# Kernel optimization log

Hardware: AMD Instinct MI355X
Metric: run time of the kernel (lower is better)

Reference implementation:

```python
import jax, jax.numpy as jnp
import numpy as np

B, S, HID = 2, 2048, 1024
H, HKV, D = 16, 8, 128
G = H // HKV  # GQA group size
EPS = 1e-6
THETA = 1000000.0


def setup_inputs() -> dict:
    key = jax.random.key(0)
    ks = jax.random.split(key, 6)
    hidden_states = jax.random.normal(ks[0], (B, S, HID), dtype=jnp.float32)
    # causal boolean mask: True = attend
    attention_mask = jnp.tril(jnp.ones((S, S), dtype=bool))[None, None]
    # RoPE tables (HF convention: freqs duplicated across both halves)
    inv_freq = 1.0 / (THETA ** (jnp.arange(0, D, 2, dtype=jnp.float32) / D))
    ang = jnp.arange(S, dtype=jnp.float32)[:, None] * inv_freq[None, :]  # [S, D/2]
    emb = jnp.concatenate([ang, ang], axis=-1)  # [S, D]
    cos, sin = jnp.cos(emb), jnp.sin(emb)
    std = 0.02
    Wq = jax.random.normal(ks[1], (HID, H * D), dtype=jnp.float32) * std
    Wk = jax.random.normal(ks[2], (HID, HKV * D), dtype=jnp.float32) * std
    Wv = jax.random.normal(ks[3], (HID, HKV * D), dtype=jnp.float32) * std
    Wo = jax.random.normal(ks[4], (H * D, HID), dtype=jnp.float32) * std
    q_norm_w = jnp.ones((D,), dtype=jnp.float32)
    k_norm_w = jnp.ones((D,), dtype=jnp.float32)
    return {"hidden_states": hidden_states, "attention_mask": attention_mask,
            "cos": cos, "sin": sin, "Wq": Wq, "Wk": Wk, "Wv": Wv, "Wo": Wo,
            "q_norm_w": q_norm_w, "k_norm_w": k_norm_w}


def _rms_norm(x, w):
    var = jnp.mean(x * x, axis=-1, keepdims=True)
    return x * jax.lax.rsqrt(var + EPS) * w


def _rotate_half(x):
    x1, x2 = jnp.split(x, 2, axis=-1)
    return jnp.concatenate([-x2, x1], axis=-1)


def reference(hidden_states, attention_mask, cos, sin, Wq, Wk, Wv, Wo, q_norm_w, k_norm_w):
    b, s, _ = hidden_states.shape
    xq = (hidden_states @ Wq).reshape(b, s, H, D).transpose(0, 2, 1, 3)    # [B,H,S,D]
    xk = (hidden_states @ Wk).reshape(b, s, HKV, D).transpose(0, 2, 1, 3)  # [B,Hkv,S,D]
    xv = (hidden_states @ Wv).reshape(b, s, HKV, D).transpose(0, 2, 1, 3)  # [B,Hkv,S,D]
    xq = _rms_norm(xq, q_norm_w)
    xk = _rms_norm(xk, k_norm_w)
    c = cos[None, None]  # [1,1,S,D]
    si = sin[None, None]
    xq = xq * c + _rotate_half(xq) * si
    xk = xk * c + _rotate_half(xk) * si
    # GQA without materializing repeated KV: group q heads per kv head
    xqg = xq.reshape(b, HKV, G, s, D)
    scale = 1.0 / jnp.sqrt(jnp.asarray(D, dtype=xq.dtype))
    scores = jnp.einsum('bkgsd,bktd->bkgst', xqg, xk) * scale  # [B,Hkv,G,S,S]
    mask = attention_mask[:, :, None]  # [1,1,1,S,S]
    scores = jnp.where(mask, scores, jnp.asarray(-jnp.inf, dtype=scores.dtype))
    probs = jax.nn.softmax(scores, axis=-1)
    out = jnp.einsum('bkgst,bktd->bkgsd', probs, xv)  # [B,Hkv,G,S,D]
    out = out.reshape(b, H, s, D).transpose(0, 2, 1, 3).reshape(b, s, H * D)
    return out @ Wo
```

## Files before the change

kernel.cpp:

```cpp
#include <hip/hip_runtime.h>
#include <stdint.h>

#define B_ 2
#define S_ 2048
#define H_ 16
#define HKV_ 8
#define D_ 128
#define EPS_ 1e-6f
#define SCALE_ 0.08838834764831845f

typedef __attribute__((ext_vector_type(8))) __bf16 bf16x8;
typedef __attribute__((ext_vector_type(4))) float f32x4;
typedef __attribute__((ext_vector_type(16))) float f32x16;

static __device__ __forceinline__ uint16_t f2b(float f) {
  uint32_t u = __builtin_bit_cast(uint32_t, f);
  u += 0x7fffu + ((u >> 16) & 1u);
  return (uint16_t)(u >> 16);
}
static __device__ __forceinline__ float b2f(uint16_t b) {
  uint32_t u = ((uint32_t)b) << 16;
  return __builtin_bit_cast(float, u);
}

typedef const __attribute__((address_space(1))) uint32_t* gas_p;
typedef __attribute__((address_space(3))) uint32_t* las_p;
static __device__ __forceinline__ void gload16(const void* g, void* l) {
  __builtin_amdgcn_global_load_lds((gas_p)g, (las_p)l, 16, 0, 0);
}

__global__ __launch_bounds__(256) void prep(const float* __restrict__ hidden,
                                            uint16_t* __restrict__ Xb,
                                            const float* __restrict__ Wq,
                                            const float* __restrict__ Wk,
                                            const float* __restrict__ Wv,
                                            const float* __restrict__ Wo,
                                            uint16_t* __restrict__ Wqt,
                                            uint16_t* __restrict__ Wkt,
                                            uint16_t* __restrict__ Wvt,
                                            uint16_t* __restrict__ Wot) {
  __shared__ float tt[32][33];
  int bid = blockIdx.x;
  if (bid < 4096) {
    int i = bid * 256 + threadIdx.x;
    float4 f = ((const float4*)hidden)[i];
    uint2 o;
    o.x = (uint32_t)f2b(f.x) | ((uint32_t)f2b(f.y) << 16);
    o.y = (uint32_t)f2b(f.z) | ((uint32_t)f2b(f.w) << 16);
    ((uint2*)Xb)[i] = o;
    return;
  }
  bid -= 4096;
  const float* src; uint16_t* dst; int K, N, bx, by;
  if (bid < 2048)       { src = Wq; dst = Wqt; K = 1024; N = 2048; bx = bid & 63; by = bid >> 6; }
  else if (bid < 3072)  { bid -= 2048; src = Wk; dst = Wkt; K = 1024; N = 1024; bx = bid & 31; by = bid >> 5; }
  else if (bid < 4096)  { bid -= 3072; src = Wv; dst = Wvt; K = 1024; N = 1024; bx = bid & 31; by = bid >> 5; }
  else                  { bid -= 4096; src = Wo; dst = Wot; K = 2048; N = 1024; bx = bid & 31; by = bid >> 5; }
  int nb = bx * 32, kb = by * 32;
  int tx = threadIdx.x & 31, ty = threadIdx.x >> 5;
  #pragma unroll
  for (int i = ty; i < 32; i += 8) tt[i][tx] = src[(size_t)(kb + i) * N + nb + tx];
  __syncthreads();
  #pragma unroll
  for (int i = ty; i < 32; i += 8) dst[(size_t)(nb + i) * K + kb + tx] = f2b(tt[tx][i]);
}

__global__ __launch_bounds__(256) void gemm_qkv(const uint16_t* __restrict__ A,
                                                const uint16_t* __restrict__ Bt,
                                                uint16_t* __restrict__ Qb,
                                                uint16_t* __restrict__ Kb,
                                                uint16_t* __restrict__ Vtb,
                                                const float* __restrict__ qw,
                                                const float* __restrict__ kw,
                                                const float* __restrict__ cosr,
                                                const float* __restrict__ sinr) {
  __shared__ uint16_t Sh[128 * 128];
  uint16_t* Al = Sh;
  uint16_t* Bl = Sh + 128 * 64;
  int tid = threadIdx.x;
  int lane = tid & 63, lr = lane & 15, g = lane >> 4;
  int w = tid >> 6, wm = w >> 1, wn = w & 1;
  int wbase = w * 64;
  int m0 = blockIdx.y * 128, n0 = blockIdx.x * 128;
  f32x4 acc[4][4] = {};
  for (int k0 = 0; k0 < 1024; k0 += 64) {
    __syncthreads();
    #pragma unroll
    for (int p = 0; p < 4; ++p) {
      int c = tid + p * 256;
      int row = c >> 3, cb = c & 7;
      int sc = (cb ^ (row & 7)) * 8;
      gload16(A + (size_t)(m0 + row) * 1024 + k0 + sc, Al + (size_t)(p * 256 + wbase) * 8);
      gload16(Bt + (size_t)(n0 + row) * 1024 + k0 + sc, Bl + (size_t)(p * 256 + wbase) * 8);
    }
    __syncthreads();
    #pragma unroll
    for (int ks = 0; ks < 2; ++ks) {
      bf16x8 af[4], bfr[4];
      #pragma unroll
      for (int mi = 0; mi < 4; ++mi) {
        int row = wm * 64 + mi * 16 + lr;
        af[mi] = *(bf16x8*)((char*)Al + row * 128 + ((ks * 64 + g * 16) ^ ((row & 7) << 4)));
      }
      #pragma unroll
      for (int ni = 0; ni < 4; ++ni) {
        int row = wn * 64 + ni * 16 + lr;
        bfr[ni] = *(bf16x8*)((char*)Bl + row * 128 + ((ks * 64 + g * 16) ^ ((row & 7) << 4)));
      }
      __builtin_amdgcn_s_setprio(1);
      #pragma unroll
      for (int mi = 0; mi < 4; ++mi)
        #pragma unroll
        for (int ni = 0; ni < 4; ++ni)
          acc[mi][ni] = __builtin_amdgcn_mfma_f32_16x16x32_bf16(af[mi], bfr[ni], acc[mi][ni], 0, 0, 0);
      __builtin_amdgcn_s_setprio(0);
    }
  }
  __syncthreads();
  uint16_t* L = Sh;
  #pragma unroll
  for (int mi = 0; mi < 4; ++mi)
    #pragma unroll
    for (int ni = 0; ni < 4; ++ni)
      #pragma unroll
      for (int e = 0; e < 4; ++e) {
        int row = wm * 64 + mi * 16 + 4 * g + e;
        int col = wn * 64 + ni * 16 + lr;
        L[row * 128 + ((((col >> 3) ^ (row & 7)) << 3) | (col & 7))] = f2b(acc[mi][ni][e]);
      }
  __syncthreads();
  int hsel = n0 >> 7;
  if (hsel < 24) {
    int row = tid >> 1, half = tid & 1;
    int gr = m0 + row, bb = gr >> 11, s = gr & 2047;
    int d0 = half * 32;
    float x[64];
    #pragma unroll
    for (int c8 = 0; c8 < 8; ++c8) {
      int j = (c8 & 3) * 8 + d0 + (c8 >> 2) * 64;
      union { bf16x8 v; uint16_t u[8]; } tmp;
      tmp.v = *(bf16x8*)(L + row * 128 + (((j >> 3) ^ (row & 7)) << 3));
      #pragma unroll
      for (int k = 0; k < 8; ++k) x[c8 * 8 + k] = b2f(tmp.u[k]);
    }
    float ss = 0.f;
    #pragma unroll
    for (int k = 0; k < 64; ++k) ss += x[k] * x[k];
    ss += __shfl_xor(ss, 1, 64);
    float rn = rsqrtf(ss * (1.0f / 128.0f) + EPS_);
    const float* wv = (hsel < 16) ? qw : kw;
    float scq = (hsel < 16) ? SCALE_ : 1.0f;
    rn *= scq;
    uint16_t* outp = (hsel < 16)
      ? Qb + (((size_t)(bb * 16 + hsel)) * 2048 + s) * 128
      : Kb + (((size_t)(bb * 8 + (hsel - 16))) * 2048 + s) * 128;
    const float* cR = cosr + s * 128;
    const float* sR = sinr + s * 128;
    #pragma unroll
    for (int c = 0; c < 4; ++c) {
      int dlo = d0 + c * 8;
      uint16_t olo[8], ohi[8];
      #pragma unroll
      for (int k = 0; k < 8; ++k) {
        int d = dlo + k;
        float x1 = x[c * 8 + k] * rn * wv[d];
        float x2 = x[32 + c * 8 + k] * rn * wv[d + 64];
        olo[k] = f2b(x1 * cR[d] - x2 * sR[d]);
        ohi[k] = f2b(x2 * cR[d + 64] + x1 * sR[d + 64]);
      }
      *(uint4*)(outp + dlo) = *(uint4*)olo;
      *(uint4*)(outp + 64 + dlo) = *(uint4*)ohi;
    }
  } else {
    int kvh = hsel - 24;
    int d0 = tid >> 1, sh = tid & 1;
    int bb = m0 >> 11, sg0 = (m0 & 2047) + sh * 64;
    union { uint16_t u[64]; uint4 q[8]; } vv;
    #pragma unroll
    for (int sl = 0; sl < 64; ++sl) {
      int srow = sh * 64 + sl;
      vv.u[sl] = L[srow * 128 + ((((d0 >> 3) ^ (srow & 7)) << 3) | (d0 & 7))];
    }
    uint16_t* vt = Vtb + (((size_t)(bb * 8 + kvh)) * 128 + d0) * 2048 + sg0;
    #pragma unroll
    for (int c = 0; c < 8; ++c) *(uint4*)(vt + c * 8) = vv.q[c];
  }
}

__global__ __launch_bounds__(256) void gemm_o(const uint16_t* __restrict__ A,
                                              const uint16_t* __restrict__ Bt,
                                              float* __restrict__ Cout,
                                              int M, int N, int K) {
  __shared__ uint16_t Al[128 * 64];
  __shared__ uint16_t Bl[64 * 64];
  int tid = threadIdx.x;
  int lane = tid & 63, lr = lane & 15, g = lane >> 4;
  int w = tid >> 6, wm = w >> 1, wn = w & 1;
  int wbase = w * 64;
  int m0 = blockIdx.y * 128, n0 = blockIdx.x * 64;
  f32x4 acc[4][2] = {};
  for (int k0 = 0; k0 < K; k0 += 64) {
    __syncthreads();
    #pragma unroll
    for (int p = 0; p < 4; ++p) {
      int c = tid + p * 256;
      int row = c >> 3, cb = c & 7;
      int sc = (cb ^ (row & 7)) * 8;
      gload16(A + (size_t)(m0 + row) * K + k0 + sc, Al + (size_t)(p * 256 + wbase) * 8);
    }
    #pragma unroll
    for (int p = 0; p < 2; ++p) {
      int c = tid + p * 256;
      int row = c >> 3, cb = c & 7;
      int sc = (cb ^ (row & 7)) * 8;
      gload16(Bt + (size_t)(n0 + row) * K + k0 + sc, Bl + (size_t)(p * 256 + wbase) * 8);
    }
    __syncthreads();
    #pragma unroll
    for (int ks = 0; ks < 2; ++ks) {
      bf16x8 af[4], bfr[2];
      #pragma unroll
      for (int mi = 0; mi < 4; ++mi) {
        int row = wm * 64 + mi * 16 + lr;
        af[mi] = *(bf16x8*)((char*)Al + row * 128 + ((ks * 64 + g * 16) ^ ((row & 7) << 4)));
      }
      #pragma unroll
      for (int ni = 0; ni < 2; ++ni) {
        int row = wn * 32 + ni * 16 + lr;
        bfr[ni] = *(bf16x8*)((char*)Bl + row * 128 + ((ks * 64 + g * 16) ^ ((row & 7) << 4)));
      }
      __builtin_amdgcn_s_setprio(1);
      #pragma unroll
      for (int mi = 0; mi < 4; ++mi)
        #pragma unroll
        for (int ni = 0; ni < 2; ++ni)
          acc[mi][ni] = __builtin_amdgcn_mfma_f32_16x16x32_bf16(af[mi], bfr[ni], acc[mi][ni], 0, 0, 0);
      __builtin_amdgcn_s_setprio(0);
    }
  }
  #pragma unroll
  for (int mi = 0; mi < 4; ++mi)
    #pragma unroll
    for (int ni = 0; ni < 2; ++ni)
      #pragma unroll
      for (int e = 0; e < 4; ++e) {
        int row = m0 + wm * 64 + mi * 16 + 4 * g + e;
        int col = n0 + wn * 32 + ni * 16 + lr;
        Cout[(size_t)row * N + col] = acc[mi][ni][e];
      }
}

#define STAGE(BUF, KB) {                                                       \
  int kb64 = (KB) * 64;                                                        \
  _Pragma("unroll") for (int p2 = 0; p2 < 4; ++p2) {                           \
    int ck = p2 * 4 + w;                                                       \
    int krow = ck * 4 + (lane >> 4);                                           \
    int kg = (lane & 15) ^ (krow & 7);                                         \
    gload16(Kg + (size_t)(kb64 + krow) * D_ + kg * 8, Kl[BUF] + ck * 512);     \
    int vrow = ck * 8 + (lane >> 3);                                           \
    int vg = (lane & 7) ^ (vrow & 7);                                          \
    gload16(Vg + (size_t)vrow * S_ + kb64 + vg * 8, Vl[BUF] + ck * 512);       \
  } }

__global__ __launch_bounds__(256, 2) void attn_kernel(const uint16_t* __restrict__ Qb,
                                                      const uint16_t* __restrict__ Kb,
                                                      const uint16_t* __restrict__ Vtg,
                                                      uint16_t* __restrict__ out) {
  __shared__ uint16_t Kl[2][64 * 128];
  __shared__ uint16_t Vl[2][128 * 64];
  int tid = threadIdx.x, lane = tid & 63, w = tid >> 6;
  int ql = lane & 31, hi = lane >> 5;
  int bi = blockIdx.x;
  int biH = bi >> 8;
  int j = bi & 255;
  int qgl = j >> 5;
  int qg = biH ? qgl : 15 - qgl;
  int rem = j & 31;
  int bkv = rem >> 1, hsel = rem & 1;
  int b = bkv >> 3, kv = bkv & 7, h = kv * 2 + hsel;
  int qt = qg * 4 + w;
  int q0 = qt * 32;
  int mykb = qt >> 1;
  int kbmax = 2 * qg + 1;
  const uint16_t* Qg = Qb + ((size_t)(b * H_ + h)) * S_ * D_;
  const uint16_t* Kg = Kb + ((size_t)(b * HKV_ + kv)) * S_ * D_;
  const uint16_t* Vg = Vtg + ((size_t)(b * HKV_ + kv)) * S_ * D_;
  bf16x8 qf[8];
  #pragma unroll
  for (int t = 0; t < 8; ++t)
    qf[t] = *(const bf16x8*)(Qg + (size_t)(q0 + ql) * D_ + t * 16 + 8 * hi);
  f32x16 O[4] = {};
  float mrun = -__builtin_inff();
  float lrun = 0.f;
  STAGE(0, 0)
  for (int kb = 0; kb <= kbmax; ++kb) {
    int cur = kb & 1;
    __syncthreads();
    if (kb < kbmax) STAGE(cur ^ 1, kb + 1)
    if (kb <= mykb) {
      const uint16_t* KlC = Kl[cur];
      const uint16_t* VlC = Vl[cur];
      bool diag = (kb == mykb);
      bool skip2 = diag && ((qt & 1) == 0);
      float p0[16], p1[16];
      {
        bf16x8 kf[8];
        #pragma unroll
        for (int t = 0; t < 8; ++t)
          kf[t] = *(const bf16x8*)(KlC + ql * 128 + (((2 * t + hi) ^ (ql & 7)) * 8));
        f32x16 acc = {};
        __builtin_amdgcn_s_setprio(1);
        #pragma unroll
        for (int t = 0; t < 8; ++t)
          acc = __builtin_amdgcn_mfma_f32_32x32x16_bf16(kf[t], qf[t], acc, 0, 0, 0);
        __builtin_amdgcn_s_setprio(0);
        #pragma unroll
        for (int r = 0; r < 16; ++r) p0[r] = acc[r];
      }
      if (!skip2) {
        bf16x8 kf[8];
        #pragma unroll
        for (int t = 0; t < 8; ++t)
          kf[t] = *(const bf16x8*)(KlC + (32 + ql) * 128 + (((2 * t + hi) ^ (ql & 7)) * 8));
        f32x16 acc = {};
        __builtin_amdgcn_s_setprio(1);
        #pragma unroll
        for (int t = 0; t < 8; ++t)
          acc = __builtin_amdgcn_mfma_f32_32x32x16_bf16(kf[t], qf[t], acc, 0, 0, 0);
        __builtin_amdgcn_s_setprio(0);
        #pragma unroll
        for (int r = 0; r < 16; ++r) p1[r] = acc[r];
      }
      if (diag && !(qt & 1)) {
        #pragma unroll
        for (int r = 0; r < 16; ++r) {
          int kk = kb * 64 + 8 * (r >> 2) + 4 * hi + (r & 3);
          if (kk > q0 + ql) p0[r] = -__builtin_inff();
        }
      }
      if (diag && (qt & 1)) {
        #pragma unroll
        for (int r = 0; r < 16; ++r) {
          int kk = kb * 64 + 32 + 8 * (r >> 2) + 4 * hi + (r & 3);
          if (kk > q0 + ql) p1[r] = -__builtin_inff();
        }
      }
      float m8[8];
      #pragma unroll
      for (int i = 0; i < 8; ++i) m8[i] = fmaxf(p0[i], p0[i + 8]);
      if (!skip2) {
        #pragma unroll
        for (int i = 0; i < 8; ++i) m8[i] = fmaxf(m8[i], fmaxf(p1[i], p1[i + 8]));
      }
      float m4a = fmaxf(m8[0], m8[4]), m4b = fmaxf(m8[1], m8[5]);
      float m4c = fmaxf(m8[2], m8[6]), m4d = fmaxf(m8[3], m8[7]);
      float pmax = fmaxf(fmaxf(m4a, m4b), fmaxf(m4c, m4d));
      pmax = fmaxf(pmax, __shfl_xor(pmax, 32, 64));
      if (__any(pmax > mrun + 8.f)) {
        float mnew = fmaxf(mrun, pmax);
        float rs = __expf(mrun - mnew);
        lrun *= rs;
        #pragma unroll
        for (int r = 0; r < 16; ++r) {
          float rr = __shfl(rs, (r & 3) + 8 * (r >> 2) + 4 * hi, 64);
          #pragma unroll
          for (int dt = 0; dt < 4; ++dt) O[dt][r] *= rr;
        }
        mrun = mnew;
      }
      float ls = 0.f;
      union PW { uint32_t w[4]; bf16x8 v; } pa0, pa1;
      #pragma unroll
      for (int r = 0; r < 16; ++r) { p0[r] = __expf(p0[r] - mrun); ls += p0[r]; }
      {
        uint32_t uu[4][2];
        #pragma unroll
        for (int T = 0; T < 4; ++T) {
          asm("v_cvt_pk_bf16_f32 %0, %1, %2" : "=v"(uu[T][0]) : "v"(p0[4 * T]), "v"(p0[4 * T + 1]));
          asm("v_cvt_pk_bf16_f32 %0, %1, %2" : "=v"(uu[T][1]) : "v"(p0[4 * T + 2]), "v"(p0[4 * T + 3]));
        }
        uint32_t a = uu[0][0], bb2 = uu[1][0];
        asm("v_permlane32_swap_b32 %0, %1" : "+v"(a), "+v"(bb2));
        uint32_t c = uu[0][1], d = uu[1][1];
        asm("v_permlane32_swap_b32 %0, %1" : "+v"(c), "+v"(d));
        pa0.w[0] = a; pa0.w[1] = c; pa0.w[2] = bb2; pa0.w[3] = d;
        uint32_t a2 = uu[2][0], b2 = uu[3][0];
        asm("v_permlane32_swap_b32 %0, %1" : "+v"(a2), "+v"(b2));
        uint32_t c2 = uu[2][1], d2 = uu[3][1];
        asm("v_permlane32_swap_b32 %0, %1" : "+v"(c2), "+v"(d2));
        pa1.w[0] = a2; pa1.w[1] = c2; pa1.w[2] = b2; pa1.w[3] = d2;
      }
      __builtin_amdgcn_s_setprio(1);
      #pragma unroll
      for (int dt = 0; dt < 4; ++dt) {
        bf16x8 v0 = *(const bf16x8*)(VlC + (dt * 32 + ql) * 64 + (((0 + hi) ^ (ql & 7)) * 8));
        bf16x8 v1 = *(const bf16x8*)(VlC + (dt * 32 + ql) * 64 + (((2 + hi) ^ (ql & 7)) * 8));
        O[dt] = __builtin_amdgcn_mfma_f32_32x32x16_bf16(pa0.v, v0, O[dt], 0, 0, 0);
        O[dt] = __builtin_amdgcn_mfma_f32_32x32x16_bf16(pa1.v, v1, O[dt], 0, 0, 0);
      }
      __builtin_amdgcn_s_setprio(0);
      if (!skip2) {
        union PW pa2, pa3;
        #pragma unroll
        for (int r = 0; r < 16; ++r) { p1[r] = __expf(p1[r] - mrun); ls += p1[r]; }
        {
          uint32_t uu[4][2];
          #pragma unroll
          for (int T = 0; T < 4; ++T) {
            asm("v_cvt_pk_bf16_f32 %0, %1, %2" : "=v"(uu[T][0]) : "v"(p1[4 * T]), "v"(p1[4 * T + 1]));
            asm("v_cvt_pk_bf16_f32 %0, %1, %2" : "=v"(uu[T][1]) : "v"(p1[4 * T + 2]), "v"(p1[4 * T + 3]));
          }
          uint32_t a = uu[0][0], bb2 = uu[1][0];
          asm("v_permlane32_swap_b32 %0, %1" : "+v"(a), "+v"(bb2));
          uint32_t c = uu[0][1], d = uu[1][1];
          asm("v_permlane32_swap_b32 %0, %1" : "+v"(c), "+v"(d));
          pa2.w[0] = a; pa2.w[1] = c; pa2.w[2] = bb2; pa2.w[3] = d;
          uint32_t a2 = uu[2][0], b2 = uu[3][0];
          asm("v_permlane32_swap_b32 %0, %1" : "+v"(a2), "+v"(b2));
          uint32_t c2 = uu[2][1], d2 = uu[3][1];
          asm("v_permlane32_swap_b32 %0, %1" : "+v"(c2), "+v"(d2));
          pa3.w[0] = a2; pa3.w[1] = c2; pa3.w[2] = b2; pa3.w[3] = d2;
        }
        __builtin_amdgcn_s_setprio(1);
        #pragma unroll
        for (int dt = 0; dt < 4; ++dt) {
          bf16x8 v2 = *(const bf16x8*)(VlC + (dt * 32 + ql) * 64 + (((4 + hi) ^ (ql & 7)) * 8));
          bf16x8 v3 = *(const bf16x8*)(VlC + (dt * 32 + ql) * 64 + (((6 + hi) ^ (ql & 7)) * 8));
          O[dt] = __builtin_amdgcn_mfma_f32_32x32x16_bf16(pa2.v, v2, O[dt], 0, 0, 0);
          O[dt] = __builtin_amdgcn_mfma_f32_32x32x16_bf16(pa3.v, v3, O[dt], 0, 0, 0);
        }
        __builtin_amdgcn_s_setprio(0);
      }
      ls += __shfl_xor(ls, 32, 64);
      lrun += ls;
    }
  }
  float linv = 1.0f / lrun;
  #pragma unroll
  for (int r = 0; r < 16; ++r) {
    int qrl = (r & 3) + 8 * (r >> 2) + 4 * hi;
    float lr_ = __shfl(linv, qrl, 64);
    #pragma unroll
    for (int dt = 0; dt < 4; ++dt) {
      size_t o = ((size_t)(b * S_ + q0 + qrl)) * 2048 + h * 128 + dt * 32 + ql;
      out[o] = f2b(O[dt][r] * lr_);
    }
  }
}

extern "C" void kernel_launch(void* const* d_in, const int* in_sizes, int n_in,
                              void* d_out, int out_size, void* d_ws, size_t ws_size,
                              hipStream_t stream) {
  const float* hidden = (const float*)d_in[0];
  const float* cosr = (const float*)d_in[2];
  const float* sinr = (const float*)d_in[3];
  const float* Wq = (const float*)d_in[4];
  const float* Wk = (const float*)d_in[5];
  const float* Wv = (const float*)d_in[6];
  const float* Wo = (const float*)d_in[7];
  const float* qw = (const float*)d_in[8];
  const float* kw = (const float*)d_in[9];

  uint16_t* p = (uint16_t*)d_ws;
  uint16_t* Xb   = p; p += (size_t)4096 * 1024;
  uint16_t* Wqt  = p; p += (size_t)2048 * 1024;
  uint16_t* Wkt  = p; p += (size_t)1024 * 1024;
  uint16_t* Wvt  = p; p += (size_t)1024 * 1024;
  uint16_t* Wot  = p; p += (size_t)1024 * 2048;
  uint16_t* Qbuf = p; p += (size_t)B_ * H_ * S_ * D_;
  uint16_t* Kbuf = p; p += (size_t)B_ * HKV_ * S_ * D_;
  uint16_t* Vtb  = p; p += (size_t)B_ * HKV_ * S_ * D_;
  uint16_t* attn = p; p += (size_t)4096 * 2048;

  prep<<<10240, 256, 0, stream>>>(hidden, Xb, Wq, Wk, Wv, Wo, Wqt, Wkt, Wvt, Wot);
  gemm_qkv<<<dim3(32, 32), 256, 0, stream>>>(Xb, Wqt, Qbuf, Kbuf, Vtb, qw, kw, cosr, sinr);
  attn_kernel<<<512, 256, 0, stream>>>(Qbuf, Kbuf, Vtb, attn);
  gemm_o<<<dim3(16, 32), 256, 0, stream>>>(attn, Wot, (float*)d_out, 4096, 1024, 2048);
}
```

Measured before the change: 174.9 us.

## Pre-pack K/V into MFMA fragment order and drop LDS staging in attention

```diff
diff --git a/kernel.cpp b/kernel.cpp
--- a/kernel.cpp
+++ b/kernel.cpp
@@ -8,6 +8,7 @@
 #define D_ 128
 #define EPS_ 1e-6f
 #define SCALE_ 0.08838834764831845f
+#define KVSTRIDE_ 262144
 
 typedef __attribute__((ext_vector_type(8))) __bf16 bf16x8;
 typedef __attribute__((ext_vector_type(4))) float f32x4;
@@ -68,8 +69,8 @@
 __global__ __launch_bounds__(256) void gemm_qkv(const uint16_t* __restrict__ A,
                                                 const uint16_t* __restrict__ Bt,
                                                 uint16_t* __restrict__ Qb,
-                                                uint16_t* __restrict__ Kb,
-                                                uint16_t* __restrict__ Vtb,
+                                                uint16_t* __restrict__ Kp,
+                                                uint16_t* __restrict__ Vp,
                                                 const float* __restrict__ qw,
                                                 const float* __restrict__ kw,
                                                 const float* __restrict__ cosr,
@@ -137,9 +138,9 @@
     float x[64];
     #pragma unroll
     for (int c8 = 0; c8 < 8; ++c8) {
-      int j = (c8 & 3) * 8 + d0 + (c8 >> 2) * 64;
+      int jj = (c8 & 3) * 8 + d0 + (c8 >> 2) * 64;
       union { bf16x8 v; uint16_t u[8]; } tmp;
-      tmp.v = *(bf16x8*)(L + row * 128 + (((j >> 3) ^ (row & 7)) << 3));
+      tmp.v = *(bf16x8*)(L + row * 128 + (((jj >> 3) ^ (row & 7)) << 3));
       #pragma unroll
       for (int k = 0; k < 8; ++k) x[c8 * 8 + k] = b2f(tmp.u[k]);
     }
@@ -151,25 +152,46 @@
     const float* wv = (hsel < 16) ? qw : kw;
     float scq = (hsel < 16) ? SCALE_ : 1.0f;
     rn *= scq;
-    uint16_t* outp = (hsel < 16)
-      ? Qb + (((size_t)(bb * 16 + hsel)) * 2048 + s) * 128
-      : Kb + (((size_t)(bb * 8 + (hsel - 16))) * 2048 + s) * 128;
     const float* cR = cosr + s * 128;
     const float* sR = sinr + s * 128;
-    #pragma unroll
-    for (int c = 0; c < 4; ++c) {
-      int dlo = d0 + c * 8;
-      uint16_t olo[8], ohi[8];
-      #pragma unroll
-      for (int k = 0; k < 8; ++k) {
-        int d = dlo + k;
-        float x1 = x[c * 8 + k] * rn * wv[d];
-        float x2 = x[32 + c * 8 + k] * rn * wv[d + 64];
-        olo[k] = f2b(x1 * cR[d] - x2 * sR[d]);
-        ohi[k] = f2b(x2 * cR[d + 64] + x1 * sR[d + 64]);
-      }
-      *(uint4*)(outp + dlo) = *(uint4*)olo;
-      *(uint4*)(outp + 64 + dlo) = *(uint4*)ohi;
+    if (hsel < 16) {
+      uint16_t* outp = Qb + (((size_t)(bb * 16 + hsel)) * 2048 + s) * 128;
+      #pragma unroll
+      for (int c = 0; c < 4; ++c) {
+        int dlo = d0 + c * 8;
+        uint16_t olo[8], ohi[8];
+        #pragma unroll
+        for (int k = 0; k < 8; ++k) {
+          int d = dlo + k;
+          float x1 = x[c * 8 + k] * rn * wv[d];
+          float x2 = x[32 + c * 8 + k] * rn * wv[d + 64];
+          olo[k] = f2b(x1 * cR[d] - x2 * sR[d]);
+          ohi[k] = f2b(x2 * cR[d + 64] + x1 * sR[d + 64]);
+        }
+        *(uint4*)(outp + dlo) = *(uint4*)olo;
+        *(uint4*)(outp + 64 + dlo) = *(uint4*)ohi;
+      }
+    } else {
+      uint16_t* kp = Kp + (size_t)(bb * 8 + (hsel - 16)) * KVSTRIDE_;
+      int kb32 = s >> 5, sl = s & 31;
+      #pragma unroll
+      for (int c = 0; c < 4; ++c) {
+        int dlo = d0 + c * 8;
+        uint16_t olo[8], ohi[8];
+        #pragma unroll
+        for (int k = 0; k < 8; ++k) {
+          int d = dlo + k;
+          float x1 = x[c * 8 + k] * rn * wv[d];
+          float x2 = x[32 + c * 8 + k] * rn * wv[d + 64];
+          olo[k] = f2b(x1 * cR[d] - x2 * sR[d]);
+          ohi[k] = f2b(x2 * cR[d + 64] + x1 * sR[d + 64]);
+        }
+        int ta = dlo >> 4, ha = (dlo >> 3) & 1;
+        *(uint4*)(kp + (((size_t)kb32 * 8 + ta) * 64 + ha * 32 + sl) * 8) = *(uint4*)olo;
+        int dhi = dlo + 64;
+        int tb = dhi >> 4, hb = (dhi >> 3) & 1;
+        *(uint4*)(kp + (((size_t)kb32 * 8 + tb) * 64 + hb * 32 + sl) * 8) = *(uint4*)ohi;
+      }
     }
   } else {
     int kvh = hsel - 24;
@@ -181,9 +203,14 @@
       int srow = sh * 64 + sl;
       vv.u[sl] = L[srow * 128 + ((((d0 >> 3) ^ (srow & 7)) << 3) | (d0 & 7))];
     }
-    uint16_t* vt = Vtb + (((size_t)(bb * 8 + kvh)) * 128 + d0) * 2048 + sg0;
-    #pragma unroll
-    for (int c = 0; c < 8; ++c) *(uint4*)(vt + c * 8) = vv.q[c];
+    uint16_t* vp = Vp + (size_t)(bb * 8 + kvh) * KVSTRIDE_;
+    int dt = d0 >> 5, qlv = d0 & 31;
+    #pragma unroll
+    for (int c = 0; c < 8; ++c) {
+      int s8 = sg0 + c * 8;
+      int kb64 = s8 >> 6, j = (s8 & 63) >> 4, hh = (s8 >> 3) & 1;
+      *(uint4*)(vp + ((((size_t)kb64 * 16) + dt * 4 + j) * 64 + hh * 32 + qlv) * 8) = vv.q[c];
+    }
   }
 }
 
@@ -250,41 +277,21 @@
       }
 }
 
-#define STAGE(BUF, KB) {                                                       \
-  int kb64 = (KB) * 64;                                                        \
-  _Pragma("unroll") for (int p2 = 0; p2 < 4; ++p2) {                           \
-    int ck = p2 * 4 + w;                                                       \
-    int krow = ck * 4 + (lane >> 4);                                           \
-    int kg = (lane & 15) ^ (krow & 7);                                         \
-    gload16(Kg + (size_t)(kb64 + krow) * D_ + kg * 8, Kl[BUF] + ck * 512);     \
-    int vrow = ck * 8 + (lane >> 3);                                           \
-    int vg = (lane & 7) ^ (vrow & 7);                                          \
-    gload16(Vg + (size_t)vrow * S_ + kb64 + vg * 8, Vl[BUF] + ck * 512);       \
-  } }
-
-__global__ __launch_bounds__(256, 2) void attn_kernel(const uint16_t* __restrict__ Qb,
-                                                      const uint16_t* __restrict__ Kb,
-                                                      const uint16_t* __restrict__ Vtg,
-                                                      uint16_t* __restrict__ out) {
-  __shared__ uint16_t Kl[2][64 * 128];
-  __shared__ uint16_t Vl[2][128 * 64];
-  int tid = threadIdx.x, lane = tid & 63, w = tid >> 6;
-  int ql = lane & 31, hi = lane >> 5;
-  int bi = blockIdx.x;
-  int biH = bi >> 8;
-  int j = bi & 255;
-  int qgl = j >> 5;
-  int qg = biH ? qgl : 15 - qgl;
-  int rem = j & 31;
-  int bkv = rem >> 1, hsel = rem & 1;
-  int b = bkv >> 3, kv = bkv & 7, h = kv * 2 + hsel;
-  int qt = qg * 4 + w;
-  int q0 = qt * 32;
-  int mykb = qt >> 1;
-  int kbmax = 2 * qg + 1;
+__global__ __launch_bounds__(64, 2) void attn_kernel(const uint16_t* __restrict__ Qb,
+                                                     const uint16_t* __restrict__ Kp,
+                                                     const uint16_t* __restrict__ Vp,
+                                                     uint16_t* __restrict__ out) {
+  int lane = threadIdx.x & 63, ql = lane & 31, hi = lane >> 5;
+  int wid = blockIdx.x;
+  int x = wid & 7, rest = wid >> 3;
+  int gsel = rest & 1, hsel = (rest >> 1) & 1, qidx = rest >> 2;
+  int gkv = gsel * 8 + x;
+  int b = gkv >> 3, kv = gkv & 7, h = kv * 2 + hsel;
+  int qt = 63 - qidx;
+  int q0 = qt * 32, mykb = qt >> 1;
   const uint16_t* Qg = Qb + ((size_t)(b * H_ + h)) * S_ * D_;
-  const uint16_t* Kg = Kb + ((size_t)(b * HKV_ + kv)) * S_ * D_;
-  const uint16_t* Vg = Vtg + ((size_t)(b * HKV_ + kv)) * S_ * D_;
+  const uint16_t* Kpg = Kp + (size_t)(b * HKV_ + kv) * KVSTRIDE_;
+  const uint16_t* Vpg = Vp + (size_t)(b * HKV_ + kv) * KVSTRIDE_;
   bf16x8 qf[8];
   #pragma unroll
   for (int t = 0; t < 8; ++t)
@@ -292,148 +299,151 @@
   f32x16 O[4] = {};
   float mrun = -__builtin_inff();
   float lrun = 0.f;
-  STAGE(0, 0)
-  for (int kb = 0; kb <= kbmax; ++kb) {
-    int cur = kb & 1;
-    __syncthreads();
-    if (kb < kbmax) STAGE(cur ^ 1, kb + 1)
-    if (kb <= mykb) {
-      const uint16_t* KlC = Kl[cur];
-      const uint16_t* VlC = Vl[cur];
-      bool diag = (kb == mykb);
-      bool skip2 = diag && ((qt & 1) == 0);
-      float p0[16], p1[16];
-      {
-        bf16x8 kf[8];
-        #pragma unroll
-        for (int t = 0; t < 8; ++t)
-          kf[t] = *(const bf16x8*)(KlC + ql * 128 + (((2 * t + hi) ^ (ql & 7)) * 8));
-        f32x16 acc = {};
-        __builtin_amdgcn_s_setprio(1);
-        #pragma unroll
-        for (int t = 0; t < 8; ++t)
-          acc = __builtin_amdgcn_mfma_f32_32x32x16_bf16(kf[t], qf[t], acc, 0, 0, 0);
-        __builtin_amdgcn_s_setprio(0);
-        #pragma unroll
-        for (int r = 0; r < 16; ++r) p0[r] = acc[r];
-      }
-      if (!skip2) {
-        bf16x8 kf[8];
-        #pragma unroll
-        for (int t = 0; t < 8; ++t)
-          kf[t] = *(const bf16x8*)(KlC + (32 + ql) * 128 + (((2 * t + hi) ^ (ql & 7)) * 8));
-        f32x16 acc = {};
-        __builtin_amdgcn_s_setprio(1);
-        #pragma unroll
-        for (int t = 0; t < 8; ++t)
-          acc = __builtin_amdgcn_mfma_f32_32x32x16_bf16(kf[t], qf[t], acc, 0, 0, 0);
-        __builtin_amdgcn_s_setprio(0);
-        #pragma unroll
-        for (int r = 0; r < 16; ++r) p1[r] = acc[r];
-      }
-      if (diag && !(qt & 1)) {
-        #pragma unroll
-        for (int r = 0; r < 16; ++r) {
-          int kk = kb * 64 + 8 * (r >> 2) + 4 * hi + (r & 3);
-          if (kk > q0 + ql) p0[r] = -__builtin_inff();
-        }
-      }
-      if (diag && (qt & 1)) {
-        #pragma unroll
-        for (int r = 0; r < 16; ++r) {
-          int kk = kb * 64 + 32 + 8 * (r >> 2) + 4 * hi + (r & 3);
-          if (kk > q0 + ql) p1[r] = -__builtin_inff();
-        }
-      }
-      float m8[8];
-      #pragma unroll
-      for (int i = 0; i < 8; ++i) m8[i] = fmaxf(p0[i], p0[i + 8]);
-      if (!skip2) {
-        #pragma unroll
-        for (int i = 0; i < 8; ++i) m8[i] = fmaxf(m8[i], fmaxf(p1[i], p1[i + 8]));
-      }
-      float m4a = fmaxf(m8[0], m8[4]), m4b = fmaxf(m8[1], m8[5]);
-      float m4c = fmaxf(m8[2], m8[6]), m4d = fmaxf(m8[3], m8[7]);
-      float pmax = fmaxf(fmaxf(m4a, m4b), fmaxf(m4c, m4d));
-      pmax = fmaxf(pmax, __shfl_xor(pmax, 32, 64));
-      if (__any(pmax > mrun + 8.f)) {
-        float mnew = fmaxf(mrun, pmax);
-        float rs = __expf(mrun - mnew);
-        lrun *= rs;
-        #pragma unroll
-        for (int r = 0; r < 16; ++r) {
-          float rr = __shfl(rs, (r & 3) + 8 * (r >> 2) + 4 * hi, 64);
-          #pragma unroll
-          for (int dt = 0; dt < 4; ++dt) O[dt][r] *= rr;
-        }
-        mrun = mnew;
-      }
-      float ls = 0.f;
-      union PW { uint32_t w[4]; bf16x8 v; } pa0, pa1;
-      #pragma unroll
-      for (int r = 0; r < 16; ++r) { p0[r] = __expf(p0[r] - mrun); ls += p0[r]; }
+  for (int kb = 0; kb <= mykb; ++kb) {
+    bool diag = (kb == mykb);
+    bool skip2 = diag && ((qt & 1) == 0);
+    const uint16_t* Kb64 = Kpg + (size_t)kb * 8192;
+    const uint16_t* Vb64 = Vpg + (size_t)kb * 8192;
+    float p0[16], p1[16];
+    {
+      bf16x8 kf[8];
+      #pragma unroll
+      for (int t = 0; t < 8; ++t)
+        kf[t] = *(const bf16x8*)(Kb64 + (t * 64 + lane) * 8);
+      f32x16 acc = {};
+      __builtin_amdgcn_s_setprio(1);
+      #pragma unroll
+      for (int t = 0; t < 8; ++t)
+        acc = __builtin_amdgcn_mfma_f32_32x32x16_bf16(kf[t], qf[t], acc, 0, 0, 0);
+      __builtin_amdgcn_s_setprio(0);
+      #pragma unroll
+      for (int r = 0; r < 16; ++r) p0[r] = acc[r];
+    }
+    if (!skip2) {
+      bf16x8 kf[8];
+      #pragma unroll
+      for (int t = 0; t < 8; ++t)
+        kf[t] = *(const bf16x8*)(Kb64 + 4096 + (t * 64 + lane) * 8);
+      f32x16 acc = {};
+      __builtin_amdgcn_s_setprio(1);
+      #pragma unroll
+      for (int t = 0; t < 8; ++t)
+        acc = __builtin_amdgcn_mfma_f32_32x32x16_bf16(kf[t], qf[t], acc, 0, 0, 0);
+      __builtin_amdgcn_s_setprio(0);
+      #pragma unroll
+      for (int r = 0; r < 16; ++r) p1[r] = acc[r];
+    }
+    bf16x8 vf[16];
+    #pragma unroll
+    for (int dt = 0; dt < 4; ++dt) {
+      vf[dt * 4 + 0] = *(const bf16x8*)(Vb64 + ((dt * 4 + 0) * 64 + lane) * 8);
+      vf[dt * 4 + 1] = *(const bf16x8*)(Vb64 + ((dt * 4 + 1) * 64 + lane) * 8);
+    }
+    if (!skip2) {
+      #pragma unroll
+      for (int dt = 0; dt < 4; ++dt) {
+        vf[dt * 4 + 2] = *(const bf16x8*)(Vb64 + ((dt * 4 + 2) * 64 + lane) * 8);
+        vf[dt * 4 + 3] = *(const bf16x8*)(Vb64 + ((dt * 4 + 3) * 64 + lane) * 8);
+      }
+    }
+    if (diag && !(qt & 1)) {
+      #pragma unroll
+      for (int r = 0; r < 16; ++r) {
+        int kk = kb * 64 + 8 * (r >> 2) + 4 * hi + (r & 3);
+        if (kk > q0 + ql) p0[r] = -__builtin_inff();
+      }
+    }
+    if (diag && (qt & 1)) {
+      #pragma unroll
+      for (int r = 0; r < 16; ++r) {
+        int kk = kb * 64 + 32 + 8 * (r >> 2) + 4 * hi + (r & 3);
+        if (kk > q0 + ql) p1[r] = -__builtin_inff();
+      }
+    }
+    float m8[8];
+    #pragma unroll
+    for (int i = 0; i < 8; ++i) m8[i] = fmaxf(p0[i], p0[i + 8]);
+    if (!skip2) {
+      #pragma unroll
+      for (int i = 0; i < 8; ++i) m8[i] = fmaxf(m8[i], fmaxf(p1[i], p1[i + 8]));
+    }
+    float m4a = fmaxf(m8[0], m8[4]), m4b = fmaxf(m8[1], m8[5]);
+    float m4c = fmaxf(m8[2], m8[6]), m4d = fmaxf(m8[3], m8[7]);
+    float pmax = fmaxf(fmaxf(m4a, m4b), fmaxf(m4c, m4d));
+    pmax = fmaxf(pmax, __shfl_xor(pmax, 32, 64));
+    if (__any(pmax > mrun + 8.f)) {
+      float mnew = fmaxf(mrun, pmax);
+      float rs = __expf(mrun - mnew);
+      lrun *= rs;
+      #pragma unroll
+      for (int r = 0; r < 16; ++r) {
+        float rr = __shfl(rs, (r & 3) + 8 * (r >> 2) + 4 * hi, 64);
+        #pragma unroll
+        for (int dt = 0; dt < 4; ++dt) O[dt][r] *= rr;
+      }
+      mrun = mnew;
+    }
+    float ls = 0.f;
+    union PW { uint32_t w[4]; bf16x8 v; } pa0, pa1;
+    #pragma unroll
+    for (int r = 0; r < 16; ++r) { p0[r] = __expf(p0[r] - mrun); ls += p0[r]; }
+    {
+      uint32_t uu[4][2];
+      #pragma unroll
+      for (int T = 0; T < 4; ++T) {
+        asm("v_cvt_pk_bf16_f32 %0, %1, %2" : "=v"(uu[T][0]) : "v"(p0[4 * T]), "v"(p0[4 * T + 1]));
+        asm("v_cvt_pk_bf16_f32 %0, %1, %2" : "=v"(uu[T][1]) : "v"(p0[4 * T + 2]), "v"(p0[4 * T + 3]));
+      }
+      uint32_t a = uu[0][0], bb2 = uu[1][0];
+      asm("v_permlane32_swap_b32 %0, %1" : "+v"(a), "+v"(bb2));
+      uint32_t c = uu[0][1], d = uu[1][1];
+      asm("v_permlane32_swap_b32 %0, %1" : "+v"(c), "+v"(d));
+      pa0.w[0] = a; pa0.w[1] = c; pa0.w[2] = bb2; pa0.w[3] = d;
+      uint32_t a2 = uu[2][0], b2 = uu[3][0];
+      asm("v_permlane32_swap_b32 %0, %1" : "+v"(a2), "+v"(b2));
+      uint32_t c2 = uu[2][1], d2 = uu[3][1];
+      asm("v_permlane32_swap_b32 %0, %1" : "+v"(c2), "+v"(d2));
+      pa1.w[0] = a2; pa1.w[1] = c2; pa1.w[2] = b2; pa1.w[3] = d2;
+    }
+    __builtin_amdgcn_s_setprio(1);
+    #pragma unroll
+    for (int dt = 0; dt < 4; ++dt) {
+      O[dt] = __builtin_amdgcn_mfma_f32_32x32x16_bf16(pa0.v, vf[dt * 4 + 0], O[dt], 0, 0, 0);
+      O[dt] = __builtin_amdgcn_mfma_f32_32x32x16_bf16(pa1.v, vf[dt * 4 + 1], O[dt], 0, 0, 0);
+    }
+    __builtin_amdgcn_s_setprio(0);
+    if (!skip2) {
+      union PW pa2, pa3;
+      #pragma unroll
+      for (int r = 0; r < 16; ++r) { p1[r] = __expf(p1[r] - mrun); ls += p1[r]; }
       {
         uint32_t uu[4][2];
         #pragma unroll
         for (int T = 0; T < 4; ++T) {
-          asm("v_cvt_pk_bf16_f32 %0, %1, %2" : "=v"(uu[T][0]) : "v"(p0[4 * T]), "v"(p0[4 * T + 1]));
-          asm("v_cvt_pk_bf16_f32 %0, %1, %2" : "=v"(uu[T][1]) : "v"(p0[4 * T + 2]), "v"(p0[4 * T + 3]));
+          asm("v_cvt_pk_bf16_f32 %0, %1, %2" : "=v"(uu[T][0]) : "v"(p1[4 * T]), "v"(p1[4 * T + 1]));
+          asm("v_cvt_pk_bf16_f32 %0, %1, %2" : "=v"(uu[T][1]) : "v"(p1[4 * T + 2]), "v"(p1[4 * T + 3]));
         }
         uint32_t a = uu[0][0], bb2 = uu[1][0];
         asm("v_permlane32_swap_b32 %0, %1" : "+v"(a), "+v"(bb2));
         uint32_t c = uu[0][1], d = uu[1][1];
         asm("v_permlane32_swap_b32 %0, %1" : "+v"(c), "+v"(d));
-        pa0.w[0] = a; pa0.w[1] = c; pa0.w[2] = bb2; pa0.w[3] = d;
+        pa2.w[0] = a; pa2.w[1] = c; pa2.w[2] = bb2; pa2.w[3] = d;
         uint32_t a2 = uu[2][0], b2 = uu[3][0];
         asm("v_permlane32_swap_b32 %0, %1" : "+v"(a2), "+v"(b2));
         uint32_t c2 = uu[2][1], d2 = uu[3][1];
         asm("v_permlane32_swap_b32 %0, %1" : "+v"(c2), "+v"(d2));
-        pa1.w[0] = a2; pa1.w[1] = c2; pa1.w[2] = b2; pa1.w[3] = d2;
+        pa3.w[0] = a2; pa3.w[1] = c2; pa3.w[2] = b2; pa3.w[3] = d2;
       }
       __builtin_amdgcn_s_setprio(1);
       #pragma unroll
       for (int dt = 0; dt < 4; ++dt) {
-        bf16x8 v0 = *(const bf16x8*)(VlC + (dt * 32 + ql) * 64 + (((0 + hi) ^ (ql & 7)) * 8));
-        bf16x8 v1 = *(const bf16x8*)(VlC + (dt * 32 + ql) * 64 + (((2 + hi) ^ (ql & 7)) * 8));
-        O[dt] = __builtin_amdgcn_mfma_f32_32x32x16_bf16(pa0.v, v0, O[dt], 0, 0, 0);
-        O[dt] = __builtin_amdgcn_mfma_f32_32x32x16_bf16(pa1.v, v1, O[dt], 0, 0, 0);
+        O[dt] = __builtin_amdgcn_mfma_f32_32x32x16_bf16(pa2.v, vf[dt * 4 + 2], O[dt], 0, 0, 0);
+        O[dt] = __builtin_amdgcn_mfma_f32_32x32x16_bf16(pa3.v, vf[dt * 4 + 3], O[dt], 0, 0, 0);
       }
       __builtin_amdgcn_s_setprio(0);
-      if (!skip2) {
-        union PW pa2, pa3;
-        #pragma unroll
-        for (int r = 0; r < 16; ++r) { p1[r] = __expf(p1[r] - mrun); ls += p1[r]; }
-        {
-          uint32_t uu[4][2];
-          #pragma unroll
-          for (int T = 0; T < 4; ++T) {
-            asm("v_cvt_pk_bf16_f32 %0, %1, %2" : "=v"(uu[T][0]) : "v"(p1[4 * T]), "v"(p1[4 * T + 1]));
-            asm("v_cvt_pk_bf16_f32 %0, %1, %2" : "=v"(uu[T][1]) : "v"(p1[4 * T + 2]), "v"(p1[4 * T + 3]));
-          }
-          uint32_t a = uu[0][0], bb2 = uu[1][0];
-          asm("v_permlane32_swap_b32 %0, %1" : "+v"(a), "+v"(bb2));
-          uint32_t c = uu[0][1], d = uu[1][1];
-          asm("v_permlane32_swap_b32 %0, %1" : "+v"(c), "+v"(d));
-          pa2.w[0] = a; pa2.w[1] = c; pa2.w[2] = bb2; pa2.w[3] = d;
-          uint32_t a2 = uu[2][0], b2 = uu[3][0];
-          asm("v_permlane32_swap_b32 %0, %1" : "+v"(a2), "+v"(b2));
-          uint32_t c2 = uu[2][1], d2 = uu[3][1];
-          asm("v_permlane32_swap_b32 %0, %1" : "+v"(c2), "+v"(d2));
-          pa3.w[0] = a2; pa3.w[1] = c2; pa3.w[2] = b2; pa3.w[3] = d2;
-        }
-        __builtin_amdgcn_s_setprio(1);
-        #pragma unroll
-        for (int dt = 0; dt < 4; ++dt) {
-          bf16x8 v2 = *(const bf16x8*)(VlC + (dt * 32 + ql) * 64 + (((4 + hi) ^ (ql & 7)) * 8));
-          bf16x8 v3 = *(const bf16x8*)(VlC + (dt * 32 + ql) * 64 + (((6 + hi) ^ (ql & 7)) * 8));
-          O[dt] = __builtin_amdgcn_mfma_f32_32x32x16_bf16(pa2.v, v2, O[dt], 0, 0, 0);
-          O[dt] = __builtin_amdgcn_mfma_f32_32x32x16_bf16(pa3.v, v3, O[dt], 0, 0, 0);
-        }
-        __builtin_amdgcn_s_setprio(0);
-      }
-      ls += __shfl_xor(ls, 32, 64);
-      lrun += ls;
-    }
+    }
+    ls += __shfl_xor(ls, 32, 64);
+    lrun += ls;
   }
   float linv = 1.0f / lrun;
   #pragma unroll
@@ -468,12 +478,12 @@
   uint16_t* Wvt  = p; p += (size_t)1024 * 1024;
   uint16_t* Wot  = p; p += (size_t)1024 * 2048;
   uint16_t* Qbuf = p; p += (size_t)B_ * H_ * S_ * D_;
-  uint16_t* Kbuf = p; p += (size_t)B_ * HKV_ * S_ * D_;
-  uint16_t* Vtb  = p; p += (size_t)B_ * HKV_ * S_ * D_;
+  uint16_t* Kpb  = p; p += (size_t)B_ * HKV_ * S_ * D_;
+  uint16_t* Vpb  = p; p += (size_t)B_ * HKV_ * S_ * D_;
   uint16_t* attn = p; p += (size_t)4096 * 2048;
 
   prep<<<10240, 256, 0, stream>>>(hidden, Xb, Wq, Wk, Wv, Wo, Wqt, Wkt, Wvt, Wot);
-  gemm_qkv<<<dim3(32, 32), 256, 0, stream>>>(Xb, Wqt, Qbuf, Kbuf, Vtb, qw, kw, cosr, sinr);
-  attn_kernel<<<512, 256, 0, stream>>>(Qbuf, Kbuf, Vtb, attn);
+  gemm_qkv<<<dim3(32, 32), 256, 0, stream>>>(Xb, Wqt, Qbuf, Kpb, Vpb, qw, kw, cosr, sinr);
+  attn_kernel<<<2048, 64, 0, stream>>>(Qbuf, Kpb, Vpb, attn);
   gemm_o<<<dim3(16, 32), 256, 0, stream>>>(attn, Wot, (float*)d_out, 4096, 1024, 2048);
 }
```

After: 213.2 us. 21.9% more time.

## Repack V into MFMA fragment layout and load directly from global memory

Applied to the files above, without the earlier changes.

```diff
diff --git a/kernel.cpp b/kernel.cpp
--- a/kernel.cpp
+++ b/kernel.cpp
@@ -8,6 +8,7 @@
 #define D_ 128
 #define EPS_ 1e-6f
 #define SCALE_ 0.08838834764831845f
+#define KVSTRIDE_ 262144
 
 typedef __attribute__((ext_vector_type(8))) __bf16 bf16x8;
 typedef __attribute__((ext_vector_type(4))) float f32x4;
@@ -137,9 +138,9 @@
     float x[64];
     #pragma unroll
     for (int c8 = 0; c8 < 8; ++c8) {
-      int j = (c8 & 3) * 8 + d0 + (c8 >> 2) * 64;
+      int jj = (c8 & 3) * 8 + d0 + (c8 >> 2) * 64;
       union { bf16x8 v; uint16_t u[8]; } tmp;
-      tmp.v = *(bf16x8*)(L + row * 128 + (((j >> 3) ^ (row & 7)) << 3));
+      tmp.v = *(bf16x8*)(L + row * 128 + (((jj >> 3) ^ (row & 7)) << 3));
       #pragma unroll
       for (int k = 0; k < 8; ++k) x[c8 * 8 + k] = b2f(tmp.u[k]);
     }
@@ -184,6 +185,23 @@
     uint16_t* vt = Vtb + (((size_t)(bb * 8 + kvh)) * 128 + d0) * 2048 + sg0;
     #pragma unroll
     for (int c = 0; c < 8; ++c) *(uint4*)(vt + c * 8) = vv.q[c];
+  }
+}
+
+__global__ __launch_bounds__(256) void vrepack(const uint16_t* __restrict__ Vt,
+                                               uint16_t* __restrict__ Vp) {
+  int bkv = blockIdx.y, p = blockIdx.x;
+  const uint16_t* src = Vt + (size_t)bkv * KVSTRIDE_;
+  uint16_t* dst = Vp + (size_t)bkv * KVSTRIDE_;
+  #pragma unroll
+  for (int i = 0; i < 16; ++i) {
+    int idx = i * 256 + threadIdx.x;
+    int d = idx >> 5, sc = p * 32 + (idx & 31);
+    int s8 = sc * 8;
+    uint4 v = *(const uint4*)(src + (size_t)d * 2048 + s8);
+    int kb64 = s8 >> 6, j = (s8 >> 4) & 3, hh = (s8 >> 3) & 1;
+    int dt = d >> 5, qlv = d & 31;
+    ((uint4*)dst)[(kb64 * 16 + dt * 4 + j) * 64 + hh * 32 + qlv] = v;
   }
 }
 
@@ -257,25 +275,21 @@
     int krow = ck * 4 + (lane >> 4);                                           \
     int kg = (lane & 15) ^ (krow & 7);                                         \
     gload16(Kg + (size_t)(kb64 + krow) * D_ + kg * 8, Kl[BUF] + ck * 512);     \
-    int vrow = ck * 8 + (lane >> 3);                                           \
-    int vg = (lane & 7) ^ (vrow & 7);                                          \
-    gload16(Vg + (size_t)vrow * S_ + kb64 + vg * 8, Vl[BUF] + ck * 512);       \
   } }
 
 __global__ __launch_bounds__(256, 2) void attn_kernel(const uint16_t* __restrict__ Qb,
                                                       const uint16_t* __restrict__ Kb,
-                                                      const uint16_t* __restrict__ Vtg,
+                                                      const uint16_t* __restrict__ Vp,
                                                       uint16_t* __restrict__ out) {
   __shared__ uint16_t Kl[2][64 * 128];
-  __shared__ uint16_t Vl[2][128 * 64];
   int tid = threadIdx.x, lane = tid & 63, w = tid >> 6;
   int ql = lane & 31, hi = lane >> 5;
   int bi = blockIdx.x;
   int biH = bi >> 8;
-  int j = bi & 255;
-  int qgl = j >> 5;
+  int j2 = bi & 255;
+  int qgl = j2 >> 5;
   int qg = biH ? qgl : 15 - qgl;
-  int rem = j & 31;
+  int rem = j2 & 31;
   int bkv = rem >> 1, hsel = rem & 1;
   int b = bkv >> 3, kv = bkv & 7, h = kv * 2 + hsel;
   int qt = qg * 4 + w;
@@ -284,7 +298,7 @@
   int kbmax = 2 * qg + 1;
   const uint16_t* Qg = Qb + ((size_t)(b * H_ + h)) * S_ * D_;
   const uint16_t* Kg = Kb + ((size_t)(b * HKV_ + kv)) * S_ * D_;
-  const uint16_t* Vg = Vtg + ((size_t)(b * HKV_ + kv)) * S_ * D_;
+  const uint16_t* Vpg = Vp + (size_t)(b * HKV_ + kv) * KVSTRIDE_;
   bf16x8 qf[8];
   #pragma unroll
   for (int t = 0; t < 8; ++t)
@@ -299,7 +313,7 @@
     if (kb < kbmax) STAGE(cur ^ 1, kb + 1)
     if (kb <= mykb) {
       const uint16_t* KlC = Kl[cur];
-      const uint16_t* VlC = Vl[cur];
+      const uint16_t* Vb64 = Vpg + (size_t)kb * 8192;
       bool diag = (kb == mykb);
       bool skip2 = diag && ((qt & 1) == 0);
       float p0[16], p1[16];
@@ -330,6 +344,19 @@
         __builtin_amdgcn_s_setprio(0);
         #pragma unroll
         for (int r = 0; r < 16; ++r) p1[r] = acc[r];
+      }
+      bf16x8 vf[16];
+      #pragma unroll
+      for (int dt = 0; dt < 4; ++dt) {
+        vf[dt * 4 + 0] = *(const bf16x8*)(Vb64 + ((dt * 4 + 0) * 64 + lane) * 8);
+        vf[dt * 4 + 1] = *(const bf16x8*)(Vb64 + ((dt * 4 + 1) * 64 + lane) * 8);
+      }
+      if (!skip2) {
+        #pragma unroll
+        for (int dt = 0; dt < 4; ++dt) {
+          vf[dt * 4 + 2] = *(const bf16x8*)(Vb64 + ((dt * 4 + 2) * 64 + lane) * 8);
+          vf[dt * 4 + 3] = *(const bf16x8*)(Vb64 + ((dt * 4 + 3) * 64 + lane) * 8);
+        }
       }
       if (diag && !(qt & 1)) {
         #pragma unroll
@@ -393,10 +420,8 @@
       __builtin_amdgcn_s_setprio(1);
       #pragma unroll
       for (int dt = 0; dt < 4; ++dt) {
-        bf16x8 v0 = *(const bf16x8*)(VlC + (dt * 32 + ql) * 64 + (((0 + hi) ^ (ql & 7)) * 8));
-        bf16x8 v1 = *(const bf16x8*)(VlC + (dt * 32 + ql) * 64 + (((2 + hi) ^ (ql & 7)) * 8));
-        O[dt] = __builtin_amdgcn_mfma_f32_32x32x16_bf16(pa0.v, v0, O[dt], 0, 0, 0);
-        O[dt] = __builtin_amdgcn_mfma_f32_32x32x16_bf16(pa1.v, v1, O[dt], 0, 0, 0);
+        O[dt] = __builtin_amdgcn_mfma_f32_32x32x16_bf16(pa0.v, vf[dt * 4 + 0], O[dt], 0, 0, 0);
+        O[dt] = __builtin_amdgcn_mfma_f32_32x32x16_bf16(pa1.v, vf[dt * 4 + 1], O[dt], 0, 0, 0);
       }
       __builtin_amdgcn_s_setprio(0);
       if (!skip2) {
@@ -424,10 +449,8 @@
         __builtin_amdgcn_s_setprio(1);
         #pragma unroll
         for (int dt = 0; dt < 4; ++dt) {
-          bf16x8 v2 = *(const bf16x8*)(VlC + (dt * 32 + ql) * 64 + (((4 + hi) ^ (ql & 7)) * 8));
-          bf16x8 v3 = *(const bf16x8*)(VlC + (dt * 32 + ql) * 64 + (((6 + hi) ^ (ql & 7)) * 8));
-          O[dt] = __builtin_amdgcn_mfma_f32_32x32x16_bf16(pa2.v, v2, O[dt], 0, 0, 0);
-          O[dt] = __builtin_amdgcn_mfma_f32_32x32x16_bf16(pa3.v, v3, O[dt], 0, 0, 0);
+          O[dt] = __builtin_amdgcn_mfma_f32_32x32x16_bf16(pa2.v, vf[dt * 4 + 2], O[dt], 0, 0, 0);
+          O[dt] = __builtin_amdgcn_mfma_f32_32x32x16_bf16(pa3.v, vf[dt * 4 + 3], O[dt], 0, 0, 0);
         }
         __builtin_amdgcn_s_setprio(0);
       }
@@ -471,9 +494,11 @@
   uint16_t* Kbuf = p; p += (size_t)B_ * HKV_ * S_ * D_;
   uint16_t* Vtb  = p; p += (size_t)B_ * HKV_ * S_ * D_;
   uint16_t* attn = p; p += (size_t)4096 * 2048;
+  uint16_t* Vpb  = Xb;
 
   prep<<<10240, 256, 0, stream>>>(hidden, Xb, Wq, Wk, Wv, Wo, Wqt, Wkt, Wvt, Wot);
   gemm_qkv<<<dim3(32, 32), 256, 0, stream>>>(Xb, Wqt, Qbuf, Kbuf, Vtb, qw, kw, cosr, sinr);
-  attn_kernel<<<512, 256, 0, stream>>>(Qbuf, Kbuf, Vtb, attn);
+  vrepack<<<dim3(8, 16), 256, 0, stream>>>(Vtb, Vpb);
+  attn_kernel<<<512, 256, 0, stream>>>(Qbuf, Kbuf, Vpb, attn);
   gemm_o<<<dim3(16, 32), 256, 0, stream>>>(attn, Wot, (float*)d_out, 4096, 1024, 2048);
 }
```

After: 174.7 us, median of 3. No clear change (-0.1%).
